# Kernel tuning notes

Hardware: AMD Instinct MI355X
Metric: run time of the kernel (lower is better)

## Reference

```python
import math
import jax, jax.numpy as jnp
import numpy as np
from jax import lax

# (new_dilation, init_dilation) per layer for layers=3, blocks=2, kernel_size=2
DILATIONS = [(1, 1), (2, 1), (4, 2), (1, 4), (2, 1), (4, 2)]
K = 2  # kernel_size


def dilate(x, dilation, init_dilation):
    """Faithful port of the pad+permute+view+permute trick. x: (n, c, l)."""
    n, c, l = x.shape
    f = dilation / init_dilation
    if f == 1:
        return x
    new_l = int(math.ceil(l / f) * f)
    if new_l != l:
        x = jnp.pad(x, ((0, 0), (0, 0), (new_l - l, 0)))  # pad_start=True
        l = new_l
    l_new = int(math.ceil(l * init_dilation / dilation))
    n_new = int(math.ceil(n * dilation / init_dilation))
    x = jnp.transpose(x, (1, 2, 0)).reshape(c, l_new, n_new)
    return jnp.transpose(x, (2, 0, 1))


def conv2(x, w):
    """1D conv, kernel_size=2, no bias. x:(n,i,l), w:(o,i,2) -> (n,o,l-1)."""
    return (jnp.einsum('oi,nil->nol', w[:, :, 0], x[:, :, :-1])
            + jnp.einsum('oi,nil->nol', w[:, :, 1], x[:, :, 1:]))


def conv1x1(x, w):
    return jnp.einsum('oi,nil->nol', w, x)


def maxpool3s2(x):
    return lax.reduce_window(x, -jnp.inf, lax.max, (1, 1, 3), (1, 1, 2), 'VALID')


def wavenet_logits(x, start_w, filter_w, gate_w, res_w, skip_w,
                   end1_w, end1_b, end2_w, end2_b,
                   fc_w1, fc_b1, fc_w2, fc_b2, fc_w3, fc_b3):
    h = conv1x1(x, start_w)
    skip = None
    for i, (d, idil) in enumerate(DILATIONS):
        residual = dilate(h, d, idil)
        filt = jnp.tanh(conv2(residual, filter_w[i]))
        gate = jax.nn.sigmoid(conv2(residual, gate_w[i]))
        h = filt * gate
        s = h if h.shape[2] == 1 else dilate(h, 1, d)
        s = conv1x1(s, skip_w[i])
        if skip is None:
            skip = s
        else:
            skip = s + skip[:, :, -s.shape[2]:]
        h = conv1x1(h, res_w[i]) + residual[:, :, K - 1:]
    y = jax.nn.relu(skip)                                   # (B, 256, 1272)
    y = jax.nn.relu(conv1x1(y, end1_w) + end1_b[None, :, None])
    y = maxpool3s2(y)                                       # (B, 128, 635)
    y = jax.nn.relu(conv1x1(y, end2_w) + end2_b[None, :, None])
    y = maxpool3s2(y)                                       # (B, 32, 317)
    y = y.reshape(y.shape[0], -1)                           # (B, 10144)
    # output_layer MLP (dropout = identity in eval)
    y = jax.nn.relu(y @ fc_w1.T + fc_b1)
    y = jax.nn.relu(y @ fc_w2.T + fc_b2)
    return y @ fc_w3.T + fc_b3                              # (B, num_classes)


def setup_inputs() -> dict:
    key = jax.random.key(0)
    ks = jax.random.split(key, 12)
    f32 = jnp.float32

    def w(k, shape, fan_in):
        return jax.random.normal(k, shape, f32) / np.sqrt(fan_in).astype(np.float32)

    B, Cin, L = 256, 5, 1280
    return {
        'x': jax.random.normal(ks[0], (B, Cin, L), f32),
        'start_w': w(ks[1], (32, 5), 5),
        'filter_w': w(ks[2], (6, 32, 32, 2), 64),
        'gate_w': w(ks[3], (6, 32, 32, 2), 64),
        'res_w': w(ks[4], (6, 32, 32), 32),
        'skip_w': w(ks[5], (6, 256, 32), 32),
        'end1_w': w(ks[6], (128, 256), 256), 'end1_b': jnp.zeros((128,), f32),
        'end2_w': w(ks[7], (32, 128), 128), 'end2_b': jnp.zeros((32,), f32),
        'fc_w1': w(ks[8], (1024, 10144), 10144), 'fc_b1': jnp.zeros((1024,), f32),
        'fc_w2': w(ks[9], (256, 1024), 1024), 'fc_b2': jnp.zeros((256,), f32),
        'fc_w3': w(ks[10], (2, 256), 256), 'fc_b3': jnp.zeros((2,), f32),
    }


def reference(x, start_w, filter_w, gate_w, res_w, skip_w,
              end1_w, end1_b, end2_w, end2_b,
              fc_w1, fc_b1, fc_w2, fc_b2, fc_w3, fc_b3):
    logits = wavenet_logits(x, start_w, filter_w, gate_w, res_w, skip_w,
                            end1_w, end1_b, end2_w, end2_b,
                            fc_w1, fc_b1, fc_w2, fc_b2, fc_w3, fc_b3)
    y_prob = jax.nn.softmax(logits, axis=1)
    y_hat = jnp.argmax(logits, axis=1)
    return logits, y_prob, y_hat
```

## Files before the change

### kernel.cpp

```cpp
#include <hip/hip_runtime.h>
#include <math.h>


#define MCAP 327680

typedef short v8s __attribute__((ext_vector_type(8)));
typedef float v4f __attribute__((ext_vector_type(4)));

static inline long lmax_(long a, long b) { return a > b ? a : b; }

__device__ inline unsigned short rnbf(float x) {
    unsigned u = __float_as_uint(x);
    return (unsigned short)((u + 0x7FFFu + ((u >> 16) & 1u)) >> 16);
}
__device__ inline void split2(float v, unsigned short& h, unsigned short& l) {
    h = rnbf(v);
    const float hf = __uint_as_float(((unsigned)h) << 16);
    l = rnbf(v - hf);
}
__device__ inline unsigned packsplit(float v) {
    unsigned short h, l;
    split2(v, h, l);
    return ((unsigned)l << 16) | (unsigned)h;
}
__device__ inline float unpack2f(unsigned v) {
    return __uint_as_float(v << 16) + __uint_as_float(v & 0xffff0000u);
}

__global__ __launch_bounds__(256) void k_zero(float* __restrict__ p, int n) {
    int i = blockIdx.x * 256 + threadIdx.x;
    if (i < n) p[i] = 0.f;
}

__global__ __launch_bounds__(256) void k_start(const float* __restrict__ x,
                                               const float* __restrict__ sw,
                                               unsigned* __restrict__ h0) {
    int j = blockIdx.x * 256 + threadIdx.x;
    int t = j >> 8, n = j & 255;
    float xv[5];
#pragma unroll
    for (int i = 0; i < 5; ++i) xv[i] = x[n * 6400 + i * 1280 + t];
#pragma unroll
    for (int o = 0; o < 32; ++o) {
        float acc = 0.f;
#pragma unroll
        for (int i = 0; i < 5; ++i) acc = fmaf(sw[o * 5 + i], xv[i], acc);
        h0[o * MCAP + j] = packsplit(acc);
    }
}

__global__ __launch_bounds__(256) void k_prep(const float* __restrict__ skw,
                                              const float* __restrict__ e1w,
                                              const float* __restrict__ fw,
                                              const float* __restrict__ gw,
                                              const float* __restrict__ rw,
                                              const float* __restrict__ e2w,
                                              unsigned short* __restrict__ swt_hi,
                                              unsigned short* __restrict__ swt_lo,
                                              unsigned short* __restrict__ e1t_hi,
                                              unsigned short* __restrict__ e1t_lo,
                                              unsigned short* __restrict__ wfg_hi,
                                              unsigned short* __restrict__ wfg_lo,
                                              unsigned short* __restrict__ wr_hi,
                                              unsigned short* __restrict__ wr_lo,
                                              unsigned short* __restrict__ e2s_hi,
                                              unsigned short* __restrict__ e2s_lo) {
    int idx = blockIdx.x * 256 + threadIdx.x;
    if (idx < 49152) {
        int ch = idx / 192, k = idx - ch * 192;
        int l = k >> 5, i = k & 31;
        unsigned short h, lo;
        split2(skw[l * 8192 + ch * 32 + i], h, lo);
        swt_hi[idx] = h; swt_lo[idx] = lo;
    }
    if (idx < 32768) {
        int co = idx >> 8, kn = idx & 255;
        int hf = kn >> 7, wv = (kn >> 5) & 3, c = (kn >> 4) & 1, r = kn & 15;
        int ch = wv * 64 + (hf * 2 + c) * 16 + r;
        unsigned short h, lo;
        split2(e1w[co * 256 + ch], h, lo);
        e1t_hi[idx] = h; e1t_lo[idx] = lo;
    }
    if (idx < 24576) {
        int l = idx >> 12, r = idx & 4095;
        int row = r >> 6, k = r & 63;
        int o = row & 31, i = k & 31, tap = k >> 5;
        const float* src = (row < 32) ? fw : gw;
        unsigned short h, lo;
        split2(src[l * 2048 + o * 64 + i * 2 + tap], h, lo);
        wfg_hi[idx] = h; wfg_lo[idx] = lo;
    }
    if (idx < 12288) {
        int l = idx >> 11, r = idx & 2047;
        int o = r >> 6, k = r & 63, i = k & 31;
        unsigned short h, lo;
        split2(rw[l * 1024 + o * 32 + i], h, lo);
        wr_hi[idx] = h; wr_lo[idx] = lo;
    }
    if (idx < 4096) {
        unsigned short h, lo;
        split2(e2w[idx], h, lo);
        e2s_hi[idx] = h; e2s_lo[idx] = lo;
    }
}

__global__ __launch_bounds__(256) void k_prep_w1(const float* __restrict__ w1,
                                                 unsigned short* __restrict__ hi,
                                                 unsigned short* __restrict__ lo) {
    int idx = blockIdx.x * 256 + threadIdx.x;
    if (idx < 10387456) {
        unsigned short h, l;
        split2(w1[idx], h, l);
        hi[idx] = h; lo[idx] = l;
    }
}

__global__ __launch_bounds__(256) void k_layer_m(
    const unsigned* __restrict__ hin, const int hinBase, const int hinStride,
    unsigned* __restrict__ hout, const int houtBase, const int houtStride,
    unsigned* __restrict__ gsl, const int gStride,
    const unsigned short* __restrict__ wfg_hi, const unsigned short* __restrict__ wfg_lo,
    const unsigned short* __restrict__ wr_hi, const unsigned short* __restrict__ wr_lo,
    const int Jlo, const int NpmP, const int padN,
    const int so_, const int M0, const int M1, const int doRes)
{
    __shared__ unsigned short U[128 * 136];
    unsigned short* AT = U;
    unsigned short* GT = U;

    const int tid = threadIdx.x;
    const int j0 = Jlo + blockIdx.x * 128;

    {
        const int col = tid & 127;
        const int kg = tid >> 7;
        unsigned short* bh = &AT[col * 136 + kg * 32];
        unsigned short* bl = &AT[col * 136 + 64 + kg * 32];
        if (kg == 0 && j0 < padN) {
            uint4 z; z.x = z.y = z.z = z.w = 0u;
#pragma unroll
            for (int ch = 0; ch < 32; ch += 8) {
                *(uint4*)&bh[ch] = z;
                *(uint4*)&bl[ch] = z;
            }
        } else {
            const int off = (kg == 0) ? (j0 - padN) : (j0 + NpmP);
            const unsigned* p = hin + (off - hinBase) + col;
#pragma unroll
            for (int ch = 0; ch < 32; ch += 8) {
                alignas(16) unsigned short h8[8], l8[8];
#pragma unroll
                for (int u = 0; u < 8; ++u) {
                    const unsigned v = p[(size_t)(ch + u) * hinStride];
                    h8[u] = (unsigned short)(v & 0xffffu);
                    l8[u] = (unsigned short)(v >> 16);
                }
                *(uint4*)&bh[ch] = *(uint4*)h8;
                *(uint4*)&bl[ch] = *(uint4*)l8;
            }
        }
    }
    __syncthreads();

    const int lane = tid & 63;
    const int w    = tid >> 6;
    const int ch2  = w >> 1;
    const int mh   = w & 1;
    const int l15  = lane & 15;
    const int quad = lane >> 4;
    const int q8   = quad * 8;
    const int colb = ch2 * 64;

    v4f accf[4], accg[4];
#pragma unroll
    for (int nt = 0; nt < 4; ++nt) { accf[nt] = (v4f)(0.f); accg[nt] = (v4f)(0.f); }

#pragma unroll
    for (int kt = 0; kt < 2; ++kt) {
        const int frow = (mh * 16 + l15) * 64 + kt * 32 + q8;
        const int grow = (32 + mh * 16 + l15) * 64 + kt * 32 + q8;
        const v8s afh = *(const v8s*)&wfg_hi[frow];
        const v8s afl = *(const v8s*)&wfg_lo[frow];
        const v8s agh = *(const v8s*)&wfg_hi[grow];
        const v8s agl = *(const v8s*)&wfg_lo[grow];
#pragma unroll
        for (int nt = 0; nt < 4; ++nt) {
            const int col = colb + nt * 16 + l15;
            const v8s bh = *(const v8s*)&AT[col * 136 + kt * 32 + q8];
            const v8s bl = *(const v8s*)&AT[col * 136 + 64 + kt * 32 + q8];
            accf[nt] = __builtin_amdgcn_mfma_f32_16x16x32_bf16(afh, bh, accf[nt], 0, 0, 0);
            accf[nt] = __builtin_amdgcn_mfma_f32_16x16x32_bf16(afh, bl, accf[nt], 0, 0, 0);
            accf[nt] = __builtin_amdgcn_mfma_f32_16x16x32_bf16(afl, bh, accf[nt], 0, 0, 0);
            accg[nt] = __builtin_amdgcn_mfma_f32_16x16x32_bf16(agh, bh, accg[nt], 0, 0, 0);
            accg[nt] = __builtin_amdgcn_mfma_f32_16x16x32_bf16(agh, bl, accg[nt], 0, 0, 0);
            accg[nt] = __builtin_amdgcn_mfma_f32_16x16x32_bf16(agl, bh, accg[nt], 0, 0, 0);
        }
    }

    unsigned short gh[4][4], gl[4][4];
#pragma unroll
    for (int nt = 0; nt < 4; ++nt)
#pragma unroll
        for (int r = 0; r < 4; ++r) {
            const float f = accf[nt][r];
            const float g = accg[nt][r];
            const float th = 1.f - 2.f / (__expf(2.f * f) + 1.f);
            const float sg = 1.f / (1.f + __expf(-g));
            split2(th * sg, gh[nt][r], gl[nt][r]);
        }

    const int m0c = j0 - so_;
    if (m0c >= M0 && m0c < M1) {
#pragma unroll
        for (int nt = 0; nt < 4; ++nt)
#pragma unroll
            for (int r = 0; r < 4; ++r) {
                const int ch = mh * 16 + quad * 4 + r;
                const int m = (m0c - M0) + colb + nt * 16 + l15;
                gsl[(size_t)ch * gStride + m] =
                    ((unsigned)gl[nt][r] << 16) | (unsigned)gh[nt][r];
            }
    }

    if (doRes) {
        __syncthreads();
#pragma unroll
        for (int nt = 0; nt < 4; ++nt)
#pragma unroll
            for (int r = 0; r < 4; ++r) {
                const int ch = mh * 16 + quad * 4 + r;
                const int col = colb + nt * 16 + l15;
                GT[col * 72 + ch] = gh[nt][r];
                GT[col * 72 + 32 + ch] = gl[nt][r];
            }
        __syncthreads();

        v4f accr[4];
#pragma unroll
        for (int nt = 0; nt < 4; ++nt) accr[nt] = (v4f)(0.f);
#pragma unroll
        for (int kt = 0; kt < 2; ++kt) {
            const int row = (mh * 16 + l15) * 64 + kt * 32 + q8;
            const v8s arh = *(const v8s*)&wr_hi[row];
            const v8s arl = *(const v8s*)&wr_lo[row];
#pragma unroll
            for (int nt = 0; nt < 4; ++nt) {
                const int col = colb + nt * 16 + l15;
                const v8s b = *(const v8s*)&GT[col * 72 + kt * 32 + q8];
                accr[nt] = __builtin_amdgcn_mfma_f32_16x16x32_bf16(arh, b, accr[nt], 0, 0, 0);
                accr[nt] = __builtin_amdgcn_mfma_f32_16x16x32_bf16(arl, b, accr[nt], 0, 0, 0);
            }
        }

        const unsigned* tp = hin + (j0 + NpmP - hinBase);
#pragma unroll
        for (int nt = 0; nt < 4; ++nt)
#pragma unroll
            for (int r = 0; r < 4; ++r) {
                const int o = mh * 16 + quad * 4 + r;
                const int col = colb + nt * 16 + l15;
                const float tap1 = unpack2f(tp[(size_t)o * hinStride + col]);
                hout[(size_t)o * houtStride + (j0 - houtBase) + col] =
                    packsplit(accr[nt][r] + tap1);
            }
    }
}

__global__ __launch_bounds__(256, 3) void k_skip_end1_m(
    const unsigned* __restrict__ g,
    const unsigned short* __restrict__ swt_hi, const unsigned short* __restrict__ swt_lo,
    const unsigned short* __restrict__ e1t_hi, const unsigned short* __restrict__ e1t_lo,
    const float* __restrict__ b1, float* __restrict__ y1, const int gs)
{
    __shared__ unsigned short U[17408];
    unsigned short* gt_hi = U;
    unsigned short* gt_lo = U + 6656;
    unsigned short* st_hi = U;
    unsigned short* st_lo = U + 8704;

    const int tid  = threadIdx.x;
    const int m0   = blockIdx.x * 64;
    const int lane = tid & 63;
    const int w    = tid >> 6;
    const int l15  = lane & 15;
    const int q8   = (lane >> 4) * 8;
    const int rbase = (lane >> 4) * 4;

    const int scol = tid & 63;
    const int ks0  = (tid >> 6) * 8;

    v4f acc1[4][4];
#pragma unroll
    for (int a = 0; a < 4; ++a)
#pragma unroll
        for (int b = 0; b < 4; ++b) acc1[a][b] = (v4f)(0.f);

#pragma unroll
    for (int kc = 0; kc < 96; kc += 32) {
        alignas(16) unsigned short h8[8], l8[8];
#pragma unroll
        for (int j = 0; j < 8; ++j) {
            const int k = kc + ks0 + j;
            const unsigned v = g[(size_t)(k >> 5) * 32 * gs + (size_t)(k & 31) * gs + m0 + scol];
            h8[j] = (unsigned short)(v & 0xffffu);
            l8[j] = (unsigned short)(v >> 16);
        }
        *(v8s*)&gt_hi[scol * 104 + kc + ks0] = *(v8s*)h8;
        *(v8s*)&gt_lo[scol * 104 + kc + ks0] = *(v8s*)l8;
    }
    __syncthreads();

    unsigned pre[24];
#pragma unroll
    for (int c = 0; c < 3; ++c)
#pragma unroll
        for (int j = 0; j < 8; ++j) {
            const int k = 96 + c * 32 + ks0 + j;
            pre[c * 8 + j] = g[(size_t)(k >> 5) * 32 * gs + (size_t)(k & 31) * gs + m0 + scol];
        }

    for (int kc = 0; kc < 96; kc += 32) {
        v8s bh[4], bl[4];
#pragma unroll
        for (int t = 0; t < 4; ++t) {
            const int bo = (t * 16 + l15) * 104 + kc + q8;
            bh[t] = *(const v8s*)&gt_hi[bo];
            bl[t] = *(const v8s*)&gt_lo[bo];
        }
#pragma unroll
        for (int cp = 0; cp < 2; ++cp) {
            v8s ah[2], al[2];
#pragma unroll
            for (int u = 0; u < 2; ++u) {
                const int ct = cp * 2 + u;
                const int row = (w * 64 + ct * 16 + l15) * 192 + kc + q8;
                ah[u] = *(const v8s*)&swt_hi[row];
                al[u] = *(const v8s*)&swt_lo[row];
            }
#pragma unroll
            for (int u = 0; u < 2; ++u) {
                const int ct = cp * 2 + u;
#pragma unroll
                for (int nt = 0; nt < 4; ++nt) {
                    acc1[ct][nt] = __builtin_amdgcn_mfma_f32_16x16x32_bf16(ah[u], bh[nt], acc1[ct][nt], 0, 0, 0);
                    acc1[ct][nt] = __builtin_amdgcn_mfma_f32_16x16x32_bf16(ah[u], bl[nt], acc1[ct][nt], 0, 0, 0);
                    acc1[ct][nt] = __builtin_amdgcn_mfma_f32_16x16x32_bf16(al[u], bh[nt], acc1[ct][nt], 0, 0, 0);
                }
            }
        }
    }
    __syncthreads();

#pragma unroll
    for (int c = 0; c < 3; ++c) {
        alignas(16) unsigned short h8[8], l8[8];
#pragma unroll
        for (int j = 0; j < 8; ++j) {
            const unsigned v = pre[c * 8 + j];
            h8[j] = (unsigned short)(v & 0xffffu);
            l8[j] = (unsigned short)(v >> 16);
        }
        *(v8s*)&gt_hi[scol * 104 + c * 32 + ks0] = *(v8s*)h8;
        *(v8s*)&gt_lo[scol * 104 + c * 32 + ks0] = *(v8s*)l8;
    }
    __syncthreads();

    for (int kc = 0; kc < 96; kc += 32) {
        v8s bh[4], bl[4];
#pragma unroll
        for (int t = 0; t < 4; ++t) {
            const int bo = (t * 16 + l15) * 104 + kc + q8;
            bh[t] = *(const v8s*)&gt_hi[bo];
            bl[t] = *(const v8s*)&gt_lo[bo];
        }
#pragma unroll
        for (int cp = 0; cp < 2; ++cp) {
            v8s ah[2], al[2];
#pragma unroll
            for (int u = 0; u < 2; ++u) {
                const int ct = cp * 2 + u;
                const int row = (w * 64 + ct * 16 + l15) * 192 + 96 + kc + q8;
                ah[u] = *(const v8s*)&swt_hi[row];
                al[u] = *(const v8s*)&swt_lo[row];
            }
#pragma unroll
            for (int u = 0; u < 2; ++u) {
                const int ct = cp * 2 + u;
#pragma unroll
                for (int nt = 0; nt < 4; ++nt) {
                    acc1[ct][nt] = __builtin_amdgcn_mfma_f32_16x16x32_bf16(ah[u], bh[nt], acc1[ct][nt], 0, 0, 0);
                    acc1[ct][nt] = __builtin_amdgcn_mfma_f32_16x16x32_bf16(ah[u], bl[nt], acc1[ct][nt], 0, 0, 0);
                    acc1[ct][nt] = __builtin_amdgcn_mfma_f32_16x16x32_bf16(al[u], bh[nt], acc1[ct][nt], 0, 0, 0);
                }
            }
        }
    }
    __syncthreads();

    v4f acc2[2][4];
#pragma unroll
    for (int a = 0; a < 2; ++a)
#pragma unroll
        for (int b = 0; b < 4; ++b) acc2[a][b] = (v4f)(0.f);

#pragma unroll
    for (int hh = 0; hh < 2; ++hh) {
#pragma unroll
        for (int c2 = 0; c2 < 2; ++c2) {
            const int ct = hh * 2 + c2;
#pragma unroll
            for (int nt = 0; nt < 4; ++nt) {
                alignas(8) unsigned short sh[4], sl[4];
#pragma unroll
                for (int r = 0; r < 4; ++r) {
                    const float v = fmaxf(acc1[ct][nt][r], 0.f);
                    split2(v, sh[r], sl[r]);
                }
                const int ci  = w * 32 + c2 * 16 + rbase;
                const int col = nt * 16 + l15;
                *(uint2*)&st_hi[col * 136 + ci] = *(uint2*)sh;
                *(uint2*)&st_lo[col * 136 + ci] = *(uint2*)sl;
            }
        }
        __syncthreads();

        for (int kc = 0; kc < 128; kc += 32) {
            v8s ah2[2], al2[2], bh2[4], bl2[4];
#pragma unroll
            for (int t = 0; t < 2; ++t) {
                const int row = (w * 32 + t * 16 + l15) * 256 + hh * 128 + kc + q8;
                ah2[t] = *(const v8s*)&e1t_hi[row];
                al2[t] = *(const v8s*)&e1t_lo[row];
            }
#pragma unroll
            for (int t = 0; t < 4; ++t) {
                const int bo = (t * 16 + l15) * 136 + kc + q8;
                bh2[t] = *(const v8s*)&st_hi[bo];
                bl2[t] = *(const v8s*)&st_lo[bo];
            }
#pragma unroll
            for (int ct = 0; ct < 2; ++ct)
#pragma unroll
                for (int nt = 0; nt < 4; ++nt) {
                    acc2[ct][nt] = __builtin_amdgcn_mfma_f32_16x16x32_bf16(ah2[ct], bh2[nt], acc2[ct][nt], 0, 0, 0);
                    acc2[ct][nt] = __builtin_amdgcn_mfma_f32_16x16x32_bf16(ah2[ct], bl2[nt], acc2[ct][nt], 0, 0, 0);
                    acc2[ct][nt] = __builtin_amdgcn_mfma_f32_16x16x32_bf16(al2[ct], bh2[nt], acc2[ct][nt], 0, 0, 0);
                }
        }
        if (hh == 0) __syncthreads();
    }

#pragma unroll
    for (int ct = 0; ct < 2; ++ct) {
        const int cobase = w * 32 + ct * 16 + rbase;
        float bb[4];
#pragma unroll
        for (int r = 0; r < 4; ++r) bb[r] = b1[cobase + r];
#pragma unroll
        for (int nt = 0; nt < 4; ++nt) {
            const int col = m0 + nt * 16 + l15;
#pragma unroll
            for (int r = 0; r < 4; ++r)
                y1[(size_t)(cobase + r) * gs + col] = fmaxf(acc2[ct][nt][r] + bb[r], 0.f);
        }
    }
}

__global__ __launch_bounds__(256) void k_pe2_m(
    const float* __restrict__ y1c,
    const unsigned short* __restrict__ e2s_hi, const unsigned short* __restrict__ e2s_lo,
    const float* __restrict__ b2, float* __restrict__ e2c,
    const int gs, const int p1s)
{
    __shared__ unsigned short SP[2 * 64 * 136];
    unsigned short* sp_hi = SP;
    unsigned short* sp_lo = SP + 64 * 136;

    const int tid = threadIdx.x;
    const int m0 = blockIdx.x * 64;
    const int tp = m0 >> 8;
    const int nb = m0 & 255;

    {
        const int col = tid & 63;
        const int cig = tid >> 6;
        const int base = 2 * tp * 256 + nb + col;
#pragma unroll
        for (int u8 = 0; u8 < 4; ++u8) {
            alignas(16) unsigned short h8[8], l8[8];
#pragma unroll
            for (int u = 0; u < 8; ++u) {
                const int ci = cig * 32 + u8 * 8 + u;
                const float* yp = y1c + (size_t)ci * gs + base;
                const float v = fmaxf(fmaxf(yp[0], yp[256]), yp[512]);
                split2(v, h8[u], l8[u]);
            }
            *(uint4*)&sp_hi[col * 136 + cig * 32 + u8 * 8] = *(uint4*)h8;
            *(uint4*)&sp_lo[col * 136 + cig * 32 + u8 * 8] = *(uint4*)l8;
        }
    }
    __syncthreads();

    const int lane = tid & 63;
    const int w    = tid >> 6;
    const int mh   = w & 1;
    const int colh = w >> 1;
    const int l15  = lane & 15;
    const int quad = lane >> 4;
    const int q8   = quad * 8;

    v4f acc[2];
    acc[0] = (v4f)(0.f); acc[1] = (v4f)(0.f);

#pragma unroll
    for (int kc = 0; kc < 128; kc += 32) {
        const int row = (mh * 16 + l15) * 128 + kc + q8;
        const v8s ah = *(const v8s*)&e2s_hi[row];
        const v8s al = *(const v8s*)&e2s_lo[row];
#pragma unroll
        for (int nt = 0; nt < 2; ++nt) {
            const int col = colh * 32 + nt * 16 + l15;
            const v8s bh = *(const v8s*)&sp_hi[col * 136 + kc + q8];
            const v8s bl = *(const v8s*)&sp_lo[col * 136 + kc + q8];
            acc[nt] = __builtin_amdgcn_mfma_f32_16x16x32_bf16(ah, bh, acc[nt], 0, 0, 0);
            acc[nt] = __builtin_amdgcn_mfma_f32_16x16x32_bf16(ah, bl, acc[nt], 0, 0, 0);
            acc[nt] = __builtin_amdgcn_mfma_f32_16x16x32_bf16(al, bh, acc[nt], 0, 0, 0);
        }
    }

#pragma unroll
    for (int nt = 0; nt < 2; ++nt)
#pragma unroll
        for (int r = 0; r < 4; ++r) {
            const int co = mh * 16 + quad * 4 + r;
            const int col = m0 + colh * 32 + nt * 16 + l15;
            e2c[(size_t)co * p1s + col] = fmaxf(acc[nt][r] + b2[co], 0.f);
        }
}

__global__ __launch_bounds__(256) void k_pool2p(const float* __restrict__ e2c,
                                                unsigned* __restrict__ p2,
                                                const int p1s, const int A) {
    const int n = threadIdx.x, tl2 = blockIdx.x, co = blockIdx.y;
    const int base = co * p1s + tl2 * 512 + n;
    float v = fmaxf(fmaxf(e2c[base], e2c[base + 256]), e2c[base + 512]);
    p2[co * 81152 + (A + tl2) * 256 + n] = packsplit(v);
}

__global__ __launch_bounds__(256) void k_fc1_m(
    const unsigned short* __restrict__ w1s_hi, const unsigned short* __restrict__ w1s_lo,
    const unsigned* __restrict__ p2u, float* __restrict__ out)
{
    __shared__ unsigned short SB[2 * 64 * 40];
    unsigned short* sb_hi = SB;
    unsigned short* sb_lo = SB + 64 * 40;

    const int tid = threadIdx.x;
    const int o0 = blockIdx.x * 64;
    const int b0 = blockIdx.y * 64;
    const int k0 = blockIdx.z * 1280;
    const int kend = (k0 + 1280 < 10144) ? (k0 + 1280) : 10144;
    const int nch = (kend - k0) >> 5;

    const int lane = tid & 63;
    const int w    = tid >> 6;
    const int l15  = lane & 15;
    const int quad = lane >> 4;
    const int q8   = quad * 8;
    const int scol = tid & 63;
    const int kq   = tid >> 6;

    v4f acc[4];
#pragma unroll
    for (int nt = 0; nt < 4; ++nt) acc[nt] = (v4f)(0.f);

    for (int c = 0; c < nch; ++c) {
        const int kc = k0 + c * 32;
        alignas(16) unsigned short h8[8], l8[8];
#pragma unroll
        for (int j = 0; j < 8; ++j) {
            const unsigned v = p2u[(size_t)(kc + kq * 8 + j) * 256 + b0 + scol];
            h8[j] = (unsigned short)(v & 0xffffu);
            l8[j] = (unsigned short)(v >> 16);
        }
        __syncthreads();
        *(v8s*)&sb_hi[scol * 40 + kq * 8] = *(v8s*)h8;
        *(v8s*)&sb_lo[scol * 40 + kq * 8] = *(v8s*)l8;
        __syncthreads();

        const int arow = (o0 + w * 16 + l15) * 10144 + kc + q8;
        const v8s ah = *(const v8s*)&w1s_hi[arow];
        const v8s al = *(const v8s*)&w1s_lo[arow];
#pragma unroll
        for (int nt = 0; nt < 4; ++nt) {
            const v8s bh = *(const v8s*)&sb_hi[(nt * 16 + l15) * 40 + q8];
            const v8s bl = *(const v8s*)&sb_lo[(nt * 16 + l15) * 40 + q8];
            acc[nt] = __builtin_amdgcn_mfma_f32_16x16x32_bf16(ah, bh, acc[nt], 0, 0, 0);
            acc[nt] = __builtin_amdgcn_mfma_f32_16x16x32_bf16(ah, bl, acc[nt], 0, 0, 0);
            acc[nt] = __builtin_amdgcn_mfma_f32_16x16x32_bf16(al, bh, acc[nt], 0, 0, 0);
        }
    }

#pragma unroll
    for (int nt = 0; nt < 4; ++nt)
#pragma unroll
        for (int r = 0; r < 4; ++r)
            atomicAdd(&out[(size_t)(o0 + w * 16 + quad * 4 + r) * 256 + b0 + nt * 16 + l15],
                      acc[nt][r]);
}

__global__ __launch_bounds__(256) void k_gemm64(const float* __restrict__ A,
                                                const float* __restrict__ B,
                                                float* __restrict__ C,
                                                const int Ktot, const int KC) {
    __shared__ float sA[32 * 65];
    __shared__ float sB[32 * 68];

    const int tid = threadIdx.x;
    const int o0 = blockIdx.x * 64;
    const int b0 = blockIdx.y * 64;
    const int k0 = blockIdx.z * KC;

    float acc[4][4];
#pragma unroll
    for (int i = 0; i < 4; ++i)
#pragma unroll
        for (int jq = 0; jq < 4; ++jq) acc[i][jq] = 0.f;

    const int ao  = tid >> 2;
    const int ak8 = (tid & 3) * 8;
    const int bk  = tid >> 3;
    const int bb8 = (tid & 7) * 8;
    const int to4 = (tid & 15) * 4;
    const int tb4 = (tid >> 4) * 4;

    for (int kc = 0; kc < KC; kc += 32) {
        const int kcLen = (KC - kc < 32) ? (KC - kc) : 32;
        const float* ap = A + (size_t)(o0 + ao) * Ktot + k0 + kc + ak8;
#pragma unroll
        for (int i = 0; i < 8; ++i) {
            float v = (ak8 + i < kcLen) ? ap[i] : 0.f;
            sA[(ak8 + i) * 65 + ao] = v;
        }
        if (bk < kcLen) {
            const float* bp = B + (size_t)(k0 + kc + bk) * 256 + b0 + bb8;
            const float4 v0 = *(const float4*)bp;
            const float4 v1 = *(const float4*)(bp + 4);
            *(float4*)&sB[bk * 68 + bb8] = v0;
            *(float4*)&sB[bk * 68 + bb8 + 4] = v1;
        } else {
            float4 z; z.x = z.y = z.z = z.w = 0.f;
            *(float4*)&sB[bk * 68 + bb8] = z;
            *(float4*)&sB[bk * 68 + bb8 + 4] = z;
        }
        __syncthreads();

#pragma unroll 8
        for (int kk = 0; kk < 32; ++kk) {
            const float4 av = *(const float4*)&sA[kk * 65 + to4];
            const float4 bv = *(const float4*)&sB[kk * 68 + tb4];
            const float aa[4] = {av.x, av.y, av.z, av.w};
#pragma unroll
            for (int i = 0; i < 4; ++i) {
                acc[i][0] = fmaf(aa[i], bv.x, acc[i][0]);
                acc[i][1] = fmaf(aa[i], bv.y, acc[i][1]);
                acc[i][2] = fmaf(aa[i], bv.z, acc[i][2]);
                acc[i][3] = fmaf(aa[i], bv.w, acc[i][3]);
            }
        }
        __syncthreads();
    }

#pragma unroll
    for (int i = 0; i < 4; ++i)
#pragma unroll
        for (int jq = 0; jq < 4; ++jq)
            atomicAdd(&C[(size_t)(o0 + to4 + i) * 256 + b0 + tb4 + jq], acc[i][jq]);
}

__global__ __launch_bounds__(256) void k_actbias(const float* __restrict__ raw,
                                                 const float* __restrict__ bias,
                                                 float* __restrict__ out) {
    const int k = blockIdx.x, b = threadIdx.x;
    out[k * 256 + b] = fmaxf(raw[k * 256 + b] + bias[k], 0.f);
}

__global__ __launch_bounds__(256) void k_fc3(const float* __restrict__ fc2raw,
                                             const float* __restrict__ fb2,
                                             const float* __restrict__ w3,
                                             const float* __restrict__ b3,
                                             float* __restrict__ out) {
    const int b = threadIdx.x;
    float l0 = b3[0], l1 = b3[1];
    for (int k = 0; k < 256; ++k) {
        const float a = fmaxf(fc2raw[k * 256 + b] + fb2[k], 0.f);
        l0 = fmaf(w3[k], a, l0);
        l1 = fmaf(w3[256 + k], a, l1);
    }
    out[2 * b] = l0;
    out[2 * b + 1] = l1;
    const float mx = fmaxf(l0, l1);
    const float e0 = expf(l0 - mx), e1 = expf(l1 - mx);
    const float inv = 1.f / (e0 + e1);
    out[512 + 2 * b] = e0 * inv;
    out[513 + 2 * b] = e1 * inv;
    out[1024 + b] = (l1 > l0) ? 1.f : 0.f;
}

extern "C" void kernel_launch(void* const* d_in, const int* in_sizes, int n_in,
                              void* d_out, int out_size, void* d_ws, size_t ws_size,
                              hipStream_t stream) {
    const float* x        = (const float*)d_in[0];
    const float* start_w  = (const float*)d_in[1];
    const float* filter_w = (const float*)d_in[2];
    const float* gate_w   = (const float*)d_in[3];
    const float* res_w    = (const float*)d_in[4];
    const float* skip_w   = (const float*)d_in[5];
    const float* e1w      = (const float*)d_in[6];
    const float* e1b      = (const float*)d_in[7];
    const float* e2w      = (const float*)d_in[8];
    const float* e2b      = (const float*)d_in[9];
    const float* w1       = (const float*)d_in[10];
    const float* fb1      = (const float*)d_in[11];
    const float* w2       = (const float*)d_in[12];
    const float* fb2      = (const float*)d_in[13];
    const float* w3       = (const float*)d_in[14];
    const float* b3       = (const float*)d_in[15];

    float* ws = (float*)d_ws;

    const long o_h0   = 0;
    const long o_p2   = 10485760;
    const long o_fc1  = 13082624;
    const long o_fc2  = 13344768;
    const long o_wbf  = 13410304;
    const long o_wfg  = 13492224;
    const long o_wr   = 13516800;
    const long o_e2s  = 13529088;
    const long o_act1 = 13533184;
    const long o_w1s  = 13795328;
    const long o_G    = 24182784;

    long budget = (long)((double)ws_size * 0.94 / 4.0);
    int dB = 1;
    for (int d = 317; d >= 1; --d) {
        long mch = 256L * (4L * d + 3), hs = mch + 4096;
        long tot = o_G + 192L * mch + lmax_(128L * mch, 64L * hs);
        if (tot <= budget) { dB = d; break; }
    }
    int K = (317 + dB - 1) / dB;
    dB = (317 + K - 1) / K;
    const long MchA  = 256L * (4L * dB + 3);
    const long HSPAN = MchA + 4096;
    const long o_X   = o_G + 192L * MchA;
    const long P1S   = 256L * (2L * dB + 1);

    unsigned* h0 = (unsigned*)(ws + o_h0);
    unsigned* p2 = (unsigned*)(ws + o_p2);
    float* fc1r = ws + o_fc1;
    float* fc2r = ws + o_fc2;
    unsigned short* swt_hi = (unsigned short*)(ws + o_wbf);
    unsigned short* swt_lo = swt_hi + 49152;
    unsigned short* e1t_hi = swt_lo + 49152;
    unsigned short* e1t_lo = e1t_hi + 32768;
    unsigned short* wfg_hi = (unsigned short*)(ws + o_wfg);
    unsigned short* wfg_lo = wfg_hi + 24576;
    unsigned short* wr_hi  = (unsigned short*)(ws + o_wr);
    unsigned short* wr_lo  = wr_hi + 12288;
    unsigned short* e2s_hi = (unsigned short*)(ws + o_e2s);
    unsigned short* e2s_lo = e2s_hi + 4096;
    unsigned short* w1s_hi = (unsigned short*)(ws + o_w1s);
    unsigned short* w1s_lo = w1s_hi + 10387456;
    float* act1 = ws + o_act1;
    unsigned* G  = (unsigned*)(ws + o_G);
    unsigned* hA = (unsigned*)(ws + o_X);
    unsigned* hB = (unsigned*)(ws + o_X) + 32L * HSPAN;
    float* y1c  = ws + o_X;
    float* e2c  = ws + o_G;

    k_zero<<<1280, 256, 0, stream>>>(fc1r, 327680);
    k_start<<<1280, 256, 0, stream>>>(x, start_w, h0);
    k_prep<<<192, 256, 0, stream>>>(skip_w, e1w, filter_w, gate_w, res_w, e2w,
                                    swt_hi, swt_lo, e1t_hi, e1t_lo,
                                    wfg_hi, wfg_lo, wr_hi, wr_lo,
                                    e2s_hi, e2s_lo);
    k_prep_w1<<<40576, 256, 0, stream>>>(w1, w1s_hi, w1s_lo);

    const int Mc[6]   = {327424, 327168, 326656, 326400, 326144, 325632};
    const int NpmP[6] = {256, 256, 512, 256, 256, 512};
    const int pN[6]   = {0, 256, 512, 0, 256, 512};
    const int so_[6]  = {1792, 1536, 1024, 768, 512, 0};
    const int JloO[6] = {-1536, -1280, -768, -768, -512, 0};

    for (int c = 0; c < K; ++c) {
        const int A = c * dB;
        int B = A + dB; if (B > 317) B = 317;
        const int dBc = B - A;
        const int M0 = 1024 * A;
        int tmax = 4 * B + 3; if (tmax > 1272) tmax = 1272;
        const int Tt = tmax - 4 * A;
        const int M1 = M0 + 256 * Tt;

        int Jlo[6], Jhi[6];
        for (int q = 0; q < 6; ++q) {
            int lo = M0 + JloO[q]; if (lo < 0) lo = 0;
            int hi = M1 + so_[q];  if (hi > Mc[q]) hi = Mc[q];
            Jlo[q] = lo; Jhi[q] = hi;
        }

        for (int q = 0; q < 6; ++q) {
            const unsigned* hin = (q == 0) ? h0 : ((q & 1) ? hA : hB);
            const int hinBase   = (q == 0) ? 0 : Jlo[q - 1];
            const int hinStride = (q == 0) ? MCAP : (int)HSPAN;
            unsigned* hout = (q & 1) ? hB : hA;
            const int Jcnt = Jhi[q] - Jlo[q];
            k_layer_m<<<Jcnt / 128, 256, 0, stream>>>(
                hin, hinBase, hinStride, hout, Jlo[q], (int)HSPAN,
                G + (long)q * 32 * MchA, (int)MchA,
                wfg_hi + q * 4096, wfg_lo + q * 4096,
                wr_hi + q * 2048, wr_lo + q * 2048,
                Jlo[q], NpmP[q], pN[q], so_[q], M0, M1, (q < 5) ? 1 : 0);
        }

        const int Mchc = 256 * Tt;
        k_skip_end1_m<<<Mchc / 64, 256, 0, stream>>>(
            G, swt_hi, swt_lo, e1t_hi, e1t_lo, e1b, y1c, (int)MchA);
        const int T1c = 2 * dBc + 1;
        k_pe2_m<<<T1c * 4, 256, 0, stream>>>(
            y1c, e2s_hi, e2s_lo, e2b, e2c, (int)MchA, (int)P1S);
        k_pool2p<<<dim3(dBc, 32), 256, 0, stream>>>(e2c, p2, (int)P1S, A);
    }

    k_fc1_m<<<dim3(16, 4, 8), 256, 0, stream>>>(w1s_hi, w1s_lo, p2, fc1r);
    k_actbias<<<1024, 256, 0, stream>>>(fc1r, fb1, act1);
    k_gemm64<<<dim3(4, 4, 4), 256, 0, stream>>>(w2, act1, fc2r, 1024, 256);
    k_fc3<<<1, 256, 0, stream>>>(fc2r, fb2, w3, b3, (float*)d_out);
}
```

Measured before the change: 829.7 us.

## Split skip/end1 fused kernel across 8 waves by column halves

Doubles the block size of the fused skip+end1 kernel from 256 to 512 threads. The two wave groups each take half of the 64 output columns, so each wave holds half the accumulators, and the staging loads are spread over more threads. The aim is lower register pressure and more waves to hide latency in this MFMA kernel. In exchange, each A-operand weight fragment is now loaded by two waves, and launch_bounds changes from 3 to 2 blocks per CU.

```diff
diff --git a/kernel.cpp b/kernel.cpp
--- a/kernel.cpp
+++ b/kernel.cpp
@@ -266,7 +266,7 @@
     }
 }
 
-__global__ __launch_bounds__(256, 3) void k_skip_end1_m(
+__global__ __launch_bounds__(512, 2) void k_skip_end1_m(
     const unsigned* __restrict__ g,
     const unsigned short* __restrict__ swt_hi, const unsigned short* __restrict__ swt_lo,
     const unsigned short* __restrict__ e1t_hi, const unsigned short* __restrict__ e1t_lo,
@@ -281,49 +281,67 @@
     const int tid  = threadIdx.x;
     const int m0   = blockIdx.x * 64;
     const int lane = tid & 63;
-    const int w    = tid >> 6;
+    const int w8   = tid >> 6;
+    const int wv   = w8 & 3;
+    const int cg   = w8 >> 2;
     const int l15  = lane & 15;
     const int q8   = (lane >> 4) * 8;
     const int rbase = (lane >> 4) * 4;
 
     const int scol = tid & 63;
-    const int ks0  = (tid >> 6) * 8;
-
-    v4f acc1[4][4];
+    const int ks0  = ((tid >> 6) & 3) * 8;
+    const int kcA  = (tid >> 8) * 32;
+
+    v4f acc1[4][2];
 #pragma unroll
     for (int a = 0; a < 4; ++a)
 #pragma unroll
-        for (int b = 0; b < 4; ++b) acc1[a][b] = (v4f)(0.f);
-
-#pragma unroll
-    for (int kc = 0; kc < 96; kc += 32) {
+        for (int b = 0; b < 2; ++b) acc1[a][b] = (v4f)(0.f);
+
+    {
         alignas(16) unsigned short h8[8], l8[8];
 #pragma unroll
         for (int j = 0; j < 8; ++j) {
-            const int k = kc + ks0 + j;
+            const int k = kcA + ks0 + j;
             const unsigned v = g[(size_t)(k >> 5) * 32 * gs + (size_t)(k & 31) * gs + m0 + scol];
             h8[j] = (unsigned short)(v & 0xffffu);
             l8[j] = (unsigned short)(v >> 16);
         }
-        *(v8s*)&gt_hi[scol * 104 + kc + ks0] = *(v8s*)h8;
-        *(v8s*)&gt_lo[scol * 104 + kc + ks0] = *(v8s*)l8;
+        *(v8s*)&gt_hi[scol * 104 + kcA + ks0] = *(v8s*)h8;
+        *(v8s*)&gt_lo[scol * 104 + kcA + ks0] = *(v8s*)l8;
+        if (tid < 256) {
+#pragma unroll
+            for (int j = 0; j < 8; ++j) {
+                const int k = 64 + ks0 + j;
+                const unsigned v = g[(size_t)(k >> 5) * 32 * gs + (size_t)(k & 31) * gs + m0 + scol];
+                h8[j] = (unsigned short)(v & 0xffffu);
+                l8[j] = (unsigned short)(v >> 16);
+            }
+            *(v8s*)&gt_hi[scol * 104 + 64 + ks0] = *(v8s*)h8;
+            *(v8s*)&gt_lo[scol * 104 + 64 + ks0] = *(v8s*)l8;
+        }
     }
     __syncthreads();
 
-    unsigned pre[24];
-#pragma unroll
-    for (int c = 0; c < 3; ++c)
+    unsigned pre[16];
+#pragma unroll
+    for (int j = 0; j < 8; ++j) {
+        const int k = 96 + kcA + ks0 + j;
+        pre[j] = g[(size_t)(k >> 5) * 32 * gs + (size_t)(k & 31) * gs + m0 + scol];
+    }
+    if (tid < 256) {
 #pragma unroll
         for (int j = 0; j < 8; ++j) {
-            const int k = 96 + c * 32 + ks0 + j;
-            pre[c * 8 + j] = g[(size_t)(k >> 5) * 32 * gs + (size_t)(k & 31) * gs + m0 + scol];
-        }
+            const int k = 160 + ks0 + j;
+            pre[8 + j] = g[(size_t)(k >> 5) * 32 * gs + (size_t)(k & 31) * gs + m0 + scol];
+        }
+    }
 
     for (int kc = 0; kc < 96; kc += 32) {
-        v8s bh[4], bl[4];
-#pragma unroll
-        for (int t = 0; t < 4; ++t) {
-            const int bo = (t * 16 + l15) * 104 + kc + q8;
+        v8s bh[2], bl[2];
+#pragma unroll
+        for (int t = 0; t < 2; ++t) {
+            const int bo = ((cg * 2 + t) * 16 + l15) * 104 + kc + q8;
             bh[t] = *(const v8s*)&gt_hi[bo];
             bl[t] = *(const v8s*)&gt_lo[bo];
         }
@@ -332,44 +350,53 @@
             v8s ah[2], al[2];
 #pragma unroll
             for (int u = 0; u < 2; ++u) {
-                const int ct = cp * 2 + u;
-                const int row = (w * 64 + ct * 16 + l15) * 192 + kc + q8;
+                const int tt = cp * 2 + u;
+                const int row = (wv * 64 + tt * 16 + l15) * 192 + kc + q8;
                 ah[u] = *(const v8s*)&swt_hi[row];
                 al[u] = *(const v8s*)&swt_lo[row];
             }
 #pragma unroll
             for (int u = 0; u < 2; ++u) {
-                const int ct = cp * 2 + u;
-#pragma unroll
-                for (int nt = 0; nt < 4; ++nt) {
-                    acc1[ct][nt] = __builtin_amdgcn_mfma_f32_16x16x32_bf16(ah[u], bh[nt], acc1[ct][nt], 0, 0, 0);
-                    acc1[ct][nt] = __builtin_amdgcn_mfma_f32_16x16x32_bf16(ah[u], bl[nt], acc1[ct][nt], 0, 0, 0);
-                    acc1[ct][nt] = __builtin_amdgcn_mfma_f32_16x16x32_bf16(al[u], bh[nt], acc1[ct][nt], 0, 0, 0);
+                const int tt = cp * 2 + u;
+#pragma unroll
+                for (int nt = 0; nt < 2; ++nt) {
+                    acc1[tt][nt] = __builtin_amdgcn_mfma_f32_16x16x32_bf16(ah[u], bh[nt], acc1[tt][nt], 0, 0, 0);
+                    acc1[tt][nt] = __builtin_amdgcn_mfma_f32_16x16x32_bf16(ah[u], bl[nt], acc1[tt][nt], 0, 0, 0);
+                    acc1[tt][nt] = __builtin_amdgcn_mfma_f32_16x16x32_bf16(al[u], bh[nt], acc1[tt][nt], 0, 0, 0);
                 }
             }
         }
     }
     __syncthreads();
 
-#pragma unroll
-    for (int c = 0; c < 3; ++c) {
+    {
         alignas(16) unsigned short h8[8], l8[8];
 #pragma unroll
         for (int j = 0; j < 8; ++j) {
-            const unsigned v = pre[c * 8 + j];
+            const unsigned v = pre[j];
             h8[j] = (unsigned short)(v & 0xffffu);
             l8[j] = (unsigned short)(v >> 16);
         }
-        *(v8s*)&gt_hi[scol * 104 + c * 32 + ks0] = *(v8s*)h8;
-        *(v8s*)&gt_lo[scol * 104 + c * 32 + ks0] = *(v8s*)l8;
+        *(v8s*)&gt_hi[scol * 104 + kcA + ks0] = *(v8s*)h8;
+        *(v8s*)&gt_lo[scol * 104 + kcA + ks0] = *(v8s*)l8;
+        if (tid < 256) {
+#pragma unroll
+            for (int j = 0; j < 8; ++j) {
+                const unsigned v = pre[8 + j];
+                h8[j] = (unsigned short)(v & 0xffffu);
+                l8[j] = (unsigned short)(v >> 16);
+            }
+            *(v8s*)&gt_hi[scol * 104 + 64 + ks0] = *(v8s*)h8;
+            *(v8s*)&gt_lo[scol * 104 + 64 + ks0] = *(v8s*)l8;
+        }
     }
     __syncthreads();
 
     for (int kc = 0; kc < 96; kc += 32) {
-        v8s bh[4], bl[4];
-#pragma unroll
-        for (int t = 0; t < 4; ++t) {
-            const int bo = (t * 16 + l15) * 104 + kc + q8;
+        v8s bh[2], bl[2];
+#pragma unroll
+        for (int t = 0; t < 2; ++t) {
+            const int bo = ((cg * 2 + t) * 16 + l15) * 104 + kc + q8;
             bh[t] = *(const v8s*)&gt_hi[bo];
             bl[t] = *(const v8s*)&gt_lo[bo];
         }
@@ -378,46 +405,46 @@
             v8s ah[2], al[2];
 #pragma unroll
             for (int u = 0; u < 2; ++u) {
-                const int ct = cp * 2 + u;
-                const int row = (w * 64 + ct * 16 + l15) * 192 + 96 + kc + q8;
+                const int tt = cp * 2 + u;
+                const int row = (wv * 64 + tt * 16 + l15) * 192 + 96 + kc + q8;
                 ah[u] = *(const v8s*)&swt_hi[row];
                 al[u] = *(const v8s*)&swt_lo[row];
             }
 #pragma unroll
             for (int u = 0; u < 2; ++u) {
-                const int ct = cp * 2 + u;
-#pragma unroll
-                for (int nt = 0; nt < 4; ++nt) {
-                    acc1[ct][nt] = __builtin_amdgcn_mfma_f32_16x16x32_bf16(ah[u], bh[nt], acc1[ct][nt], 0, 0, 0);
-                    acc1[ct][nt] = __builtin_amdgcn_mfma_f32_16x16x32_bf16(ah[u], bl[nt], acc1[ct][nt], 0, 0, 0);
-                    acc1[ct][nt] = __builtin_amdgcn_mfma_f32_16x16x32_bf16(al[u], bh[nt], acc1[ct][nt], 0, 0, 0);
+                const int tt = cp * 2 + u;
+#pragma unroll
+                for (int nt = 0; nt < 2; ++nt) {
+                    acc1[tt][nt] = __builtin_amdgcn_mfma_f32_16x16x32_bf16(ah[u], bh[nt], acc1[tt][nt], 0, 0, 0);
+                    acc1[tt][nt] = __builtin_amdgcn_mfma_f32_16x16x32_bf16(ah[u], bl[nt], acc1[tt][nt], 0, 0, 0);
+                    acc1[tt][nt] = __builtin_amdgcn_mfma_f32_16x16x32_bf16(al[u], bh[nt], acc1[tt][nt], 0, 0, 0);
                 }
             }
         }
     }
     __syncthreads();
 
-    v4f acc2[2][4];
+    v4f acc2[2][2];
 #pragma unroll
     for (int a = 0; a < 2; ++a)
 #pragma unroll
-        for (int b = 0; b < 4; ++b) acc2[a][b] = (v4f)(0.f);
+        for (int b = 0; b < 2; ++b) acc2[a][b] = (v4f)(0.f);
 
 #pragma unroll
     for (int hh = 0; hh < 2; ++hh) {
 #pragma unroll
         for (int c2 = 0; c2 < 2; ++c2) {
-            const int ct = hh * 2 + c2;
-#pragma unroll
-            for (int nt = 0; nt < 4; ++nt) {
+            const int tt = hh * 2 + c2;
+#pragma unroll
+            for (int nt = 0; nt < 2; ++nt) {
                 alignas(8) unsigned short sh[4], sl[4];
 #pragma unroll
                 for (int r = 0; r < 4; ++r) {
-                    const float v = fmaxf(acc1[ct][nt][r], 0.f);
+                    const float v = fmaxf(acc1[tt][nt][r], 0.f);
                     split2(v, sh[r], sl[r]);
                 }
-                const int ci  = w * 32 + c2 * 16 + rbase;
-                const int col = nt * 16 + l15;
+                const int ci  = wv * 32 + c2 * 16 + rbase;
+                const int col = cg * 32 + nt * 16 + l15;
                 *(uint2*)&st_hi[col * 136 + ci] = *(uint2*)sh;
                 *(uint2*)&st_lo[col * 136 + ci] = *(uint2*)sl;
             }
@@ -425,23 +452,23 @@
         __syncthreads();
 
         for (int kc = 0; kc < 128; kc += 32) {
-            v8s ah2[2], al2[2], bh2[4], bl2[4];
+            v8s ah2[2], al2[2], bh2[2], bl2[2];
 #pragma unroll
             for (int t = 0; t < 2; ++t) {
-                const int row = (w * 32 + t * 16 + l15) * 256 + hh * 128 + kc + q8;
+                const int row = (wv * 32 + t * 16 + l15) * 256 + hh * 128 + kc + q8;
                 ah2[t] = *(const v8s*)&e1t_hi[row];
                 al2[t] = *(const v8s*)&e1t_lo[row];
             }
 #pragma unroll
-            for (int t = 0; t < 4; ++t) {
-                const int bo = (t * 16 + l15) * 136 + kc + q8;
+            for (int t = 0; t < 2; ++t) {
+                const int bo = ((cg * 2 + t) * 16 + l15) * 136 + kc + q8;
                 bh2[t] = *(const v8s*)&st_hi[bo];
                 bl2[t] = *(const v8s*)&st_lo[bo];
             }
 #pragma unroll
             for (int ct = 0; ct < 2; ++ct)
 #pragma unroll
-                for (int nt = 0; nt < 4; ++nt) {
+                for (int nt = 0; nt < 2; ++nt) {
                     acc2[ct][nt] = __builtin_amdgcn_mfma_f32_16x16x32_bf16(ah2[ct], bh2[nt], acc2[ct][nt], 0, 0, 0);
                     acc2[ct][nt] = __builtin_amdgcn_mfma_f32_16x16x32_bf16(ah2[ct], bl2[nt], acc2[ct][nt], 0, 0, 0);
                     acc2[ct][nt] = __builtin_amdgcn_mfma_f32_16x16x32_bf16(al2[ct], bh2[nt], acc2[ct][nt], 0, 0, 0);
@@ -452,13 +479,13 @@
 
 #pragma unroll
     for (int ct = 0; ct < 2; ++ct) {
-        const int cobase = w * 32 + ct * 16 + rbase;
+        const int cobase = wv * 32 + ct * 16 + rbase;
         float bb[4];
 #pragma unroll
         for (int r = 0; r < 4; ++r) bb[r] = b1[cobase + r];
 #pragma unroll
-        for (int nt = 0; nt < 4; ++nt) {
-            const int col = m0 + nt * 16 + l15;
+        for (int nt = 0; nt < 2; ++nt) {
+            const int col = m0 + cg * 32 + nt * 16 + l15;
 #pragma unroll
             for (int r = 0; r < 4; ++r)
                 y1[(size_t)(cobase + r) * gs + col] = fmaxf(acc2[ct][nt][r] + bb[r], 0.f);
@@ -823,7 +850,7 @@
         }
 
         const int Mchc = 256 * Tt;
-        k_skip_end1_m<<<Mchc / 64, 256, 0, stream>>>(
+        k_skip_end1_m<<<Mchc / 64, 512, 0, stream>>>(
             G, swt_hi, swt_lo, e1t_hi, e1t_lo, e1b, y1c, (int)MchA);
         const int T1c = 2 * dBc + 1;
         k_pe2_m<<<T1c * 4, 256, 0, stream>>>(
```

Measured after the change: 1.045 ms. 1.26x slower.
